# Kernel tuning notes

Hardware: AMD Instinct MI355X
Metric: run time of the kernel (lower is better)

The kernel has to match this reference:

```python
import jax, jax.numpy as jnp
import numpy as np

N, E, G = 50000, 1600000, 64
N_SPECIES, D_ATTR, D, N_RBF = 16, 16, 32, 8
CUTOFF = 5.0
SCALE, SHIFT = 1.0, 0.0


def setup_inputs() -> dict:
    key = jax.random.key(0)
    ks = jax.random.split(key, 20)

    def w(k, shape):
        fan_in = shape[-2] if len(shape) > 1 else shape[-1]
        return jax.random.normal(k, shape, dtype=jnp.float32) / np.sqrt(fan_in)

    return {
        "x": jax.random.randint(ks[0], (N, 1), 0, N_SPECIES),
        "pos": 3.0 * jax.random.normal(ks[1], (N, 3), dtype=jnp.float32),
        "edge_index": jax.random.randint(ks[2], (2, E), 0, N),
        "period_vec": 0.1 * jax.random.normal(ks[3], (E, 3), dtype=jnp.float32),
        "batch": jnp.sort(jax.random.randint(ks[4], (N,), 0, G)),
        "W_elem": w(ks[5], (N_SPECIES, D_ATTR)),
        "W0": w(ks[6], (D_ATTR, D)),
        "b0": jnp.zeros((D,), jnp.float32),
        "Wr1": w(ks[7], (3, N_RBF, D)),
        "br1": jnp.zeros((3, D), jnp.float32),
        "Wr2": w(ks[8], (3, D, D)),
        "Wmsg": w(ks[9], (3, D, D)),
        "Wattr": w(ks[10], (3, D_ATTR, D)),
        "Wself": w(ks[11], (3, D, D)),
        "bconv": jnp.zeros((3, D), jnp.float32),
        "wsh": w(ks[12], (3, 4)),
        "Wp1": w(ks[13], (D, 16)),
        "bp1": jnp.zeros((16,), jnp.float32),
        "Wp2": w(ks[14], (16, 1)),
        "bp2": jnp.zeros((1,), jnp.float32),
    }


def reference(x, pos, edge_index, period_vec, batch, W_elem, W0, b0, Wr1, br1,
              Wr2, Wmsg, Wattr, Wself, bconv, wsh, Wp1, bp1, Wp2, bp2):
    src, dst = edge_index[0], edge_index[1]

    # node_attr_layer: species embedding (gather), then first_atom_embed linear
    x_attr = W_elem[x[:, 0]]                              # [N, D_ATTR]
    h = x_attr @ W0 + b0                                  # [N, D]

    # edge_attr_layer: PBC edge vectors, lengths, l<=1 spherical harmonics
    edge_vec = pos[dst] - pos[src] + period_vec           # [E, 3]
    edge_len = jnp.linalg.norm(edge_vec, axis=-1, keepdims=True)  # [E, 1]
    unit = edge_vec / (edge_len + 1e-9)
    edge_sh = jnp.concatenate([jnp.ones_like(edge_len), unit], axis=-1)  # [E, 4]

    # edge_embedding_layer: Gaussian radial basis of edge lengths
    centers = jnp.linspace(0.0, CUTOFF, N_RBF, dtype=pos.dtype)
    gamma = jnp.asarray((N_RBF / CUTOFF) ** 2, pos.dtype)
    rbf = jnp.exp(-gamma * (edge_len - centers) ** 2)     # [E, N_RBF]

    # 3 conv layers: gather -> per-edge transform -> scatter-sum -> node update
    for i in range(3):
        rw = jax.nn.relu(rbf @ Wr1[i] + br1[i]) @ Wr2[i]  # [E, D] radial MLP
        sh_w = edge_sh @ wsh[i]                           # [E] sh mixing
        msg = (h[src] @ Wmsg[i]) * rw * sh_w[:, None]     # [E, D]
        agg = jax.ops.segment_sum(msg, dst, num_segments=N)  # [N, D]
        h = jax.nn.silu(agg + x_attr @ Wattr[i] + h @ Wself[i] + bconv[i])

    # post_conv layers
    h = jax.nn.silu(h @ Wp1 + bp1)                        # [N, 16]
    h = (h @ Wp2 + bp2)[:, 0]                             # [N] (squeeze)

    # scatter-sum pooling over graphs + affine energy scaling
    e = jax.ops.segment_sum(h, batch, num_segments=G)     # [G]
    return (e * SCALE + SHIFT)[:, None]                   # [G, 1]
```

## Files before the change

### kernel.cpp

```cpp
#include <hip/hip_runtime.h>
#include <hip/hip_fp16.h>
#include <math.h>

constexpr int N_NODES  = 50000;
constexpr int N_EDGES  = 1600000;
constexpr int G_GRAPHS = 64;
constexpr int D        = 32;
constexpr int D_ATTR   = 16;
constexpr int N_RBF    = 8;

constexpr int   TBL      = 8192;
constexpr int   TBL_ROWS = TBL + 1;
constexpr float LMAX     = 10.0f;

constexpr int BUCKET = 80;

constexpr int NT     = 64;
constexpr int NTILES = (N_NODES + NT - 1) / NT;
constexpr int TCAP   = 2432;
constexpr int EPB      = 2048;
constexpr int STHREADS = 512;
constexpr int EPV      = EPB / STHREADS;
constexpr int NBLK1    = (N_EDGES + EPB - 1) / EPB;

constexpr int NSLOT = NTILES * NT * BUCKET;

typedef unsigned int  uint4v  __attribute__((ext_vector_type(4)));
typedef unsigned int  uint2v  __attribute__((ext_vector_type(2)));

__device__ __forceinline__ float silu(float x) {
    return x / (1.0f + __expf(-x));
}
__device__ __forceinline__ float h2f_bits(unsigned short u) {
    return __half2float(__ushort_as_half(u));
}
__device__ __forceinline__ __half2 h2u(unsigned v) {
    union { unsigned u; __half2 h; } c; c.u = v; return c.h;
}

__global__ void node_init_kernel(const int* __restrict__ x,
                                 const float* __restrict__ W_elem,
                                 const float* __restrict__ W0,
                                 const float* __restrict__ b0,
                                 const float* __restrict__ Wmsg0,
                                 const float* __restrict__ Wself0,
                                 const float* __restrict__ Wattr,
                                 const float* __restrict__ bconv,
                                 __half* __restrict__ hm0,
                                 float* __restrict__ hs0,
                                 float* __restrict__ xa1,
                                 float* __restrict__ xa2,
                                 float* __restrict__ out) {
    int t = blockIdx.x * blockDim.x + threadIdx.x;
    if (t < G_GRAPHS) out[t] = 0.0f;
    int n = t >> 5, c = t & 31;
    if (n >= N_NODES) return;
    int sp = x[n];
    const float* we = W_elem + sp * D_ATTR;
    float xv = (c < D_ATTR) ? we[c] : 0.0f;
    float acc = b0[c];
#pragma unroll
    for (int a = 0; a < D_ATTR; ++a) acc += we[a] * W0[a * D + c];
    float m = 0.0f, s = 0.0f;
#pragma unroll
    for (int j = 0; j < D; ++j) {
        float hj = __shfl(acc, j, 32);
        m = fmaf(hj, Wmsg0[j * D + c], m);
        s = fmaf(hj, Wself0[j * D + c], s);
    }
    float a0 = bconv[0 * D + c], a1 = bconv[1 * D + c], a2 = bconv[2 * D + c];
#pragma unroll
    for (int j = 0; j < D_ATTR; ++j) {
        float xj = __shfl(xv, j, 32);
        a0 = fmaf(xj, Wattr[0 * D_ATTR * D + j * D + c], a0);
        a1 = fmaf(xj, Wattr[1 * D_ATTR * D + j * D + c], a1);
        a2 = fmaf(xj, Wattr[2 * D_ATTR * D + j * D + c], a2);
    }
    hm0[n * D + c] = __float2half(m);
    hs0[n * D + c] = s + a0;
    xa1[n * D + c] = a1;
    xa2[n * D + c] = a2;
}

__global__ __launch_bounds__(STHREADS) void hist_kernel(const int* __restrict__ eidx,
                                                        int* __restrict__ blk_hist) {
    __shared__ int hist[NTILES];
    int tid = threadIdx.x;
    int e0 = blockIdx.x * EPB;
    for (int i = tid; i < NTILES; i += STHREADS) hist[i] = 0;
    __syncthreads();
#pragma unroll
    for (int i = 0; i < EPV; ++i) {
        int e = e0 + tid + STHREADS * i;
        if (e < N_EDGES) atomicAdd(&hist[eidx[N_EDGES + e] >> 6], 1);
    }
    __syncthreads();
    int* dst = blk_hist + (size_t)blockIdx.x * NTILES;
    for (int t = tid; t < NTILES; t += STHREADS) dst[t] = hist[t];
}

__global__ void scan_kernel(const int* __restrict__ blk_hist,
                            int* __restrict__ blk_base,
                            int* __restrict__ tile_total) {
    int t = blockIdx.x;
    int lane = threadIdx.x;
    int run = 0;
    for (int b0 = 0; b0 < NBLK1; b0 += 64) {
        int b = b0 + lane;
        int v = (b < NBLK1) ? blk_hist[(size_t)b * NTILES + t] : 0;
        int pre = v;
#pragma unroll
        for (int o = 1; o < 64; o <<= 1) {
            int w = __shfl_up(pre, o);
            if (lane >= o) pre += w;
        }
        int excl = pre - v;
        if (b < NBLK1) blk_base[(size_t)b * NTILES + t] = run + excl;
        run += __shfl(pre, 63);
    }
    if (lane == 0) tile_total[t] = run;
}

__global__ __launch_bounds__(STHREADS) void scatter_kernel(const int* __restrict__ eidx,
                                                           const float* __restrict__ pos,
                                                           const float* __restrict__ period,
                                                           const float* __restrict__ wsh,
                                                           const int* __restrict__ blk_base,
                                                           uint4v* __restrict__ bins) {
    __shared__ int hist[NTILES];
    __shared__ int basev[NTILES];
    int tid = threadIdx.x;
    int e0 = blockIdx.x * EPB;
    const int* bb = blk_base + (size_t)blockIdx.x * NTILES;
    for (int i = tid; i < NTILES; i += STHREADS) {
        hist[i] = 0;
        basev[i] = bb[i];
    }
    __syncthreads();

    int   sarr[EPV], darr[EPV];
    float vx[EPV], vy[EPV], vz[EPV];
#pragma unroll
    for (int i = 0; i < EPV; ++i) {
        int e  = e0 + tid + STHREADS * i;
        int ec = (e < N_EDGES) ? e : (N_EDGES - 1);
        int s = eidx[ec];
        int d = eidx[N_EDGES + ec];
        sarr[i] = s;
        darr[i] = d;
        vx[i] = pos[d * 3 + 0] - pos[s * 3 + 0] + period[ec * 3 + 0];
        vy[i] = pos[d * 3 + 1] - pos[s * 3 + 1] + period[ec * 3 + 1];
        vz[i] = pos[d * 3 + 2] - pos[s * 3 + 2] + period[ec * 3 + 2];
    }
    asm volatile("" ::
        "v"(vx[0]), "v"(vx[1]), "v"(vx[2]), "v"(vx[3]),
        "v"(vy[0]), "v"(vy[1]), "v"(vy[2]), "v"(vy[3]),
        "v"(vz[0]), "v"(vz[1]), "v"(vz[2]), "v"(vz[3]),
        "v"(sarr[0]), "v"(sarr[1]), "v"(sarr[2]), "v"(sarr[3]),
        "v"(darr[0]), "v"(darr[1]), "v"(darr[2]), "v"(darr[3]));
#pragma unroll
    for (int i = 0; i < EPV; ++i) {
        int e = e0 + tid + STHREADS * i;
        if (e >= N_EDGES) continue;
        float len = sqrtf(vx[i] * vx[i] + vy[i] * vy[i] + vz[i] * vz[i]);
        float inv = 1.0f / (len + 1e-9f);
        int idx = (int)fminf(len * ((float)TBL / LMAX) + 0.5f, (float)TBL);
        float sw[3];
#pragma unroll
        for (int l = 0; l < 3; ++l)
            sw[l] = wsh[l * 4 + 0] +
                    (vx[i] * wsh[l * 4 + 1] + vy[i] * wsh[l * 4 + 2] + vz[i] * wsh[l * 4 + 3]) * inv;
        int tile = darr[i] >> 6;
        int rank = atomicAdd(&hist[tile], 1);
        int slot = basev[tile] + rank;
        if (slot < TCAP) {
            unsigned u0 = (unsigned)__half_as_ushort(__float2half(sw[0]));
            unsigned u1 = (unsigned)__half_as_ushort(__float2half(sw[1]));
            unsigned u2 = (unsigned)__half_as_ushort(__float2half(sw[2]));
            uint4v r;
            r.x = (unsigned)sarr[i] | ((unsigned)idx << 16);
            r.y = (unsigned)(darr[i] & (NT - 1));
            r.z = u0 | (u1 << 16);
            r.w = u2;
            bins[(size_t)tile * TCAP + slot] = r;
        }
    }
}

__global__ __launch_bounds__(512) void shuffle_kernel(const uint4v* __restrict__ bins,
                                                      const int* __restrict__ tile_total,
                                                      unsigned int* __restrict__ xs,
                                                      unsigned short* __restrict__ swp,
                                                      int* __restrict__ count) {
    __shared__ int lcur[NT];
    int tile = blockIdx.x;
    int tid = threadIdx.x;
    if (tid < NT) lcur[tid] = 0;
    __syncthreads();
    int cnt = tile_total[tile];
    if (cnt > TCAP) cnt = TCAP;
    const uint4v* base = bins + (size_t)tile * TCAP;
    for (int i = tid; i < cnt; i += 512) {
        uint4v r = __builtin_nontemporal_load(base + i);
        int dl = (int)(r.y & 63u);
        int slot = atomicAdd(&lcur[dl], 1);
        if (slot < BUCKET) {
            size_t g = (size_t)(tile * NT + dl) * BUCKET + slot;
            xs[g] = r.x;
            swp[0 * (size_t)NSLOT + g] = (unsigned short)(r.z & 0xFFFFu);
            swp[1 * (size_t)NSLOT + g] = (unsigned short)(r.z >> 16);
            swp[2 * (size_t)NSLOT + g] = (unsigned short)(r.w & 0xFFFFu);
        }
    }
    __syncthreads();
    if (tid < NT) {
        int node = tile * NT + tid;
        if (node < N_NODES) {
            int c = lcur[tid];
            count[node] = c < BUCKET ? c : BUCKET;
        }
    }
}

__global__ void table_kernel(const float* __restrict__ Wr1,
                             const float* __restrict__ br1,
                             const float* __restrict__ Wr2,
                             __half* __restrict__ table) {
    int t = blockIdx.x * blockDim.x + threadIdx.x;
    if (t >= 3 * TBL_ROWS) return;
    int l = t / TBL_ROWS;
    int idx = t % TBL_ROWS;
    float len = (float)idx * (LMAX / (float)TBL);
    const float gamma = (8.0f / 5.0f) * (8.0f / 5.0f);
    float rbf[N_RBF];
#pragma unroll
    for (int k = 0; k < N_RBF; ++k) {
        float dd = len - (float)k * (5.0f / 7.0f);
        rbf[k] = __expf(-gamma * dd * dd);
    }
    float out[D];
#pragma unroll
    for (int c = 0; c < D; ++c) out[c] = 0.0f;
    for (int j = 0; j < D; ++j) {
        float z = br1[l * D + j];
#pragma unroll
        for (int k = 0; k < N_RBF; ++k) z += rbf[k] * Wr1[l * N_RBF * D + k * D + j];
        z = fmaxf(z, 0.0f);
        const float* w2 = Wr2 + l * D * D + j * D;
#pragma unroll
        for (int c = 0; c < D; ++c) out[c] += z * w2[c];
    }
    __half* dst = table + ((size_t)(l * TBL_ROWS + idx)) * D;
#pragma unroll
    for (int c = 0; c < D; ++c) dst[c] = __float2half(out[c]);
}

template <int LAYER, bool NEXT>
__global__ __launch_bounds__(256, 5) void conv_kernel(const __half* __restrict__ hm,
                            const float* __restrict__ hs,
                            const unsigned int* __restrict__ xs,
                            const unsigned short* __restrict__ swp,
                            const int* __restrict__ count,
                            const __half* __restrict__ table,
                            const float* __restrict__ Wmsg_next,
                            const float* __restrict__ Wself_next,
                            const float* __restrict__ xa_next,
                            __half* __restrict__ hm_out,
                            float* __restrict__ hs_out,
                            float* __restrict__ h_final) {
    int wid = (blockIdx.x * blockDim.x + threadIdx.x) >> 6;
    int na = wid * 2;
    if (na >= N_NODES) return;
    int nb = na + 1;
    int lane = threadIdx.x & 63;
    int qw = lane >> 4;
    int q  = lane & 15;

    const unsigned* tab2 = (const unsigned*)(table + ((size_t)LAYER * TBL_ROWS) * D);
    const unsigned* hm2  = (const unsigned*)hm;
    const unsigned short* swb = swp + (size_t)LAYER * NSLOT;

    int cnta = count[na], cntb = count[nb];
    int bega = na * BUCKET, begb = nb * BUCKET;
    int enda = bega + cnta, endb = begb + cntb;
    int mx = cnta > cntb ? cnta : cntb;

    float axa = 0.0f, aya = 0.0f, axb = 0.0f, ayb = 0.0f;
    for (int k = 0; k < BUCKET; k += 32) {
        int o0a = bega + k + qw * 4, o1a = o0a + 16;
        int o0b = begb + k + qw * 4, o1b = o0b + 16;
        uint4v xa0 = __builtin_nontemporal_load((const uint4v*)(xs + o0a));
        uint4v xa1 = __builtin_nontemporal_load((const uint4v*)(xs + o1a));
        uint4v xb0 = __builtin_nontemporal_load((const uint4v*)(xs + o0b));
        uint4v xb1 = __builtin_nontemporal_load((const uint4v*)(xs + o1b));
        uint2v wa0 = __builtin_nontemporal_load((const uint2v*)(swb + o0a));
        uint2v wa1 = __builtin_nontemporal_load((const uint2v*)(swb + o1a));
        uint2v wb0 = __builtin_nontemporal_load((const uint2v*)(swb + o0b));
        uint2v wb1 = __builtin_nontemporal_load((const uint2v*)(swb + o1b));
        unsigned ua[8] = {xa0.x, xa0.y, xa0.z, xa0.w, xa1.x, xa1.y, xa1.z, xa1.w};
        unsigned ub[8] = {xb0.x, xb0.y, xb0.z, xb0.w, xb1.x, xb1.y, xb1.z, xb1.w};
        unsigned tva[8], mva[8], tvb[8], mvb[8];
#pragma unroll
        for (int j = 0; j < 8; ++j) {
            int slot = (j < 4) ? (o0a + j) : (o1a + j - 4);
            unsigned uu = (slot < enda) ? ua[j] : 0u;
            tva[j] = tab2[(int)(uu >> 16) * 16 + q];
            mva[j] = hm2[(int)(uu & 0xFFFFu) * 16 + q];
        }
#pragma unroll
        for (int j = 0; j < 8; ++j) {
            int slot = (j < 4) ? (o0b + j) : (o1b + j - 4);
            unsigned uu = (slot < endb) ? ub[j] : 0u;
            tvb[j] = tab2[(int)(uu >> 16) * 16 + q];
            mvb[j] = hm2[(int)(uu & 0xFFFFu) * 16 + q];
        }
        asm volatile("" ::
            "v"(tva[0]), "v"(tva[1]), "v"(tva[2]), "v"(tva[3]),
            "v"(tva[4]), "v"(tva[5]), "v"(tva[6]), "v"(tva[7]),
            "v"(mva[0]), "v"(mva[1]), "v"(mva[2]), "v"(mva[3]),
            "v"(mva[4]), "v"(mva[5]), "v"(mva[6]), "v"(mva[7]),
            "v"(tvb[0]), "v"(tvb[1]), "v"(tvb[2]), "v"(tvb[3]),
            "v"(tvb[4]), "v"(tvb[5]), "v"(tvb[6]), "v"(tvb[7]),
            "v"(mvb[0]), "v"(mvb[1]), "v"(mvb[2]), "v"(mvb[3]),
            "v"(mvb[4]), "v"(mvb[5]), "v"(mvb[6]), "v"(mvb[7]));
        unsigned short wva[8] = {
            (unsigned short)(wa0.x & 0xFFFFu), (unsigned short)(wa0.x >> 16),
            (unsigned short)(wa0.y & 0xFFFFu), (unsigned short)(wa0.y >> 16),
            (unsigned short)(wa1.x & 0xFFFFu), (unsigned short)(wa1.x >> 16),
            (unsigned short)(wa1.y & 0xFFFFu), (unsigned short)(wa1.y >> 16)};
        unsigned short wvb[8] = {
            (unsigned short)(wb0.x & 0xFFFFu), (unsigned short)(wb0.x >> 16),
            (unsigned short)(wb0.y & 0xFFFFu), (unsigned short)(wb0.y >> 16),
            (unsigned short)(wb1.x & 0xFFFFu), (unsigned short)(wb1.x >> 16),
            (unsigned short)(wb1.y & 0xFFFFu), (unsigned short)(wb1.y >> 16)};
#pragma unroll
        for (int j = 0; j < 8; ++j) {
            int slot = (j < 4) ? (o0a + j) : (o1a + j - 4);
            float sw = (slot < enda) ? h2f_bits(wva[j]) : 0.0f;
            float2 pf = __half22float2(__hmul2(h2u(tva[j]), h2u(mva[j])));
            axa = fmaf(pf.x, sw, axa);
            aya = fmaf(pf.y, sw, aya);
        }
#pragma unroll
        for (int j = 0; j < 8; ++j) {
            int slot = (j < 4) ? (o0b + j) : (o1b + j - 4);
            float sw = (slot < endb) ? h2f_bits(wvb[j]) : 0.0f;
            float2 pf = __half22float2(__hmul2(h2u(tvb[j]), h2u(mvb[j])));
            axb = fmaf(pf.x, sw, axb);
            ayb = fmaf(pf.y, sw, ayb);
        }
        if (k + 32 >= mx) break;
    }
    axa += __shfl_xor(axa, 16); axa += __shfl_xor(axa, 32);
    aya += __shfl_xor(aya, 16); aya += __shfl_xor(aya, 32);
    axb += __shfl_xor(axb, 16); axb += __shfl_xor(axb, 32);
    ayb += __shfl_xor(ayb, 16); ayb += __shfl_xor(ayb, 32);

    int c = lane & 31;
    float vxa = __shfl(axa, c >> 1), vya = __shfl(aya, c >> 1);
    float vxb = __shfl(axb, c >> 1), vyb = __shfl(ayb, c >> 1);
    float agga = (c & 1) ? vya : vxa;
    float aggb = (c & 1) ? vyb : vxb;
    bool hi = lane >= 32;
    int mynode = hi ? nb : na;
    float agg = hi ? aggb : agga;

    float hn = silu(agg + hs[mynode * D + c]);
    if (NEXT) {
        float m = 0.0f, s2 = 0.0f;
#pragma unroll
        for (int j = 0; j < D; ++j) {
            float hj = __shfl(hn, j, 32);
            m  = fmaf(hj, Wmsg_next[j * D + c], m);
            s2 = fmaf(hj, Wself_next[j * D + c], s2);
        }
        hm_out[mynode * D + c] = __float2half(m);
        hs_out[mynode * D + c] = s2 + xa_next[mynode * D + c];
    } else {
        h_final[mynode * D + c] = hn;
    }
}

__global__ void readout_kernel(const float* __restrict__ h,
                               const int* __restrict__ batch,
                               const float* __restrict__ Wp1,
                               const float* __restrict__ bp1,
                               const float* __restrict__ Wp2,
                               const float* __restrict__ bp2,
                               float* __restrict__ out) {
    int n = blockIdx.x * blockDim.x + threadIdx.x;
    float s = 0.0f;
    int b = -1;
    if (n < N_NODES) {
        b = batch[n];
        const float* hrow = h + n * D;
        float acc2 = bp2[0];
#pragma unroll
        for (int m = 0; m < 16; ++m) {
            float a = bp1[m];
#pragma unroll
            for (int j = 0; j < D; ++j) a += hrow[j] * Wp1[j * 16 + m];
            acc2 += silu(a) * Wp2[m];
        }
        s = acc2;
    }
    unsigned long long valid = __ballot(n < N_NODES);
    if (valid == 0ull) return;
    int firstLane = __ffsll(valid) - 1;
    int b0v = __shfl(b, firstLane);
    bool ok = (b == b0v) || (n >= N_NODES);
    if (__all(ok)) {
#pragma unroll
        for (int o = 32; o > 0; o >>= 1) s += __shfl_down(s, o);
        if ((threadIdx.x & 63) == 0) atomicAdd(out + b0v, s);
    } else {
        if (n < N_NODES) atomicAdd(out + b, s);
    }
}

extern "C" void kernel_launch(void* const* d_in, const int* in_sizes, int n_in,
                              void* d_out, int out_size, void* d_ws, size_t ws_size,
                              hipStream_t stream) {
    const int*   x      = (const int*)d_in[0];
    const float* pos    = (const float*)d_in[1];
    const int*   eidx   = (const int*)d_in[2];
    const float* period = (const float*)d_in[3];
    const int*   batch  = (const int*)d_in[4];
    const float* W_elem = (const float*)d_in[5];
    const float* W0     = (const float*)d_in[6];
    const float* b0     = (const float*)d_in[7];
    const float* Wr1    = (const float*)d_in[8];
    const float* br1    = (const float*)d_in[9];
    const float* Wr2    = (const float*)d_in[10];
    const float* Wmsg   = (const float*)d_in[11];
    const float* Wattr  = (const float*)d_in[12];
    const float* Wself  = (const float*)d_in[13];
    const float* bconv  = (const float*)d_in[14];
    const float* wsh    = (const float*)d_in[15];
    const float* Wp1    = (const float*)d_in[16];
    const float* bp1    = (const float*)d_in[17];
    const float* Wp2    = (const float*)d_in[18];
    const float* bp2    = (const float*)d_in[19];

    char* base = (char*)d_ws;
    size_t off = 0;
    auto carve = [&](size_t bytes) -> void* {
        void* p = base + off;
        off = (off + bytes + 255) & ~(size_t)255;
        return p;
    };
    __half*         hm_a        = (__half*)carve((size_t)N_NODES * D * 2);
    __half*         hm_b        = (__half*)carve((size_t)N_NODES * D * 2);
    float*          hs_a        = (float*)carve((size_t)N_NODES * D * 4);
    float*          hs_b        = (float*)carve((size_t)N_NODES * D * 4);
    float*          xa1         = (float*)carve((size_t)N_NODES * D * 4);
    float*          xa2         = (float*)carve((size_t)N_NODES * D * 4);
    float*          h_final     = (float*)carve((size_t)N_NODES * D * 4);
    unsigned int*   xs          = (unsigned int*)carve((size_t)NSLOT * 4);
    unsigned short* swp         = (unsigned short*)carve((size_t)3 * NSLOT * 2);
    uint4v*         bins        = (uint4v*)carve((size_t)NTILES * TCAP * 16);
    int*            blk_hist    = (int*)carve((size_t)NBLK1 * NTILES * 4);
    int*            blk_base    = (int*)carve((size_t)NBLK1 * NTILES * 4);
    int*            tile_total  = (int*)carve((size_t)NTILES * 4);
    int*            count       = (int*)carve((size_t)NTILES * NT * 4);
    __half*         table       = (__half*)carve((size_t)3 * TBL_ROWS * D * 2);
    (void)ws_size; (void)in_sizes; (void)n_in; (void)out_size;

    node_init_kernel<<<(N_NODES * 32 + 255) / 256, 256, 0, stream>>>(
        x, W_elem, W0, b0, Wmsg + 0 * D * D, Wself + 0 * D * D, Wattr, bconv,
        hm_a, hs_a, xa1, xa2, (float*)d_out);
    hist_kernel<<<NBLK1, STHREADS, 0, stream>>>(eidx, blk_hist);
    scan_kernel<<<NTILES, 64, 0, stream>>>(blk_hist, blk_base, tile_total);
    scatter_kernel<<<NBLK1, STHREADS, 0, stream>>>(eidx, pos, period, wsh, blk_base, bins);
    table_kernel<<<(3 * TBL_ROWS + 127) / 128, 128, 0, stream>>>(Wr1, br1, Wr2, table);
    shuffle_kernel<<<NTILES, 512, 0, stream>>>(bins, tile_total, xs, swp, count);

    int cwaves = (N_NODES + 1) / 2;
    int cgrid  = (cwaves * 64 + 255) / 256;
    conv_kernel<0, true><<<cgrid, 256, 0, stream>>>(
        hm_a, hs_a, xs, swp, count, table, Wmsg + 1 * D * D, Wself + 1 * D * D, xa1,
        hm_b, hs_b, nullptr);
    conv_kernel<1, true><<<cgrid, 256, 0, stream>>>(
        hm_b, hs_b, xs, swp, count, table, Wmsg + 2 * D * D, Wself + 2 * D * D, xa2,
        hm_a, hs_a, nullptr);
    conv_kernel<2, false><<<cgrid, 256, 0, stream>>>(
        hm_a, hs_a, xs, swp, count, table, nullptr, nullptr, nullptr,
        nullptr, nullptr, h_final);

    readout_kernel<<<(N_NODES + 255) / 256, 256, 0, stream>>>(h_final, batch, Wp1, bp1, Wp2, bp2,
                                                              (float*)d_out);
}
```

Measured before the change: 388.8 us.

## Gather table and node rows with 16-byte loads, four lanes per edge

Restructures the conv gather so each lane loads a 16-byte chunk of the table row and the message row (four lanes per edge, sixteen edges per pass) instead of 4-byte chunks with sixteen lanes per edge. Each lane now keeps eight accumulators, reduced by a shuffle tree and combined through shared memory with a block barrier. The aim is fewer, wider memory transactions per edge. In exchange it needs more registers, lowered by relaxing launch bounds from 5 to 4 blocks, and adds a __syncthreads that sits after an early return for out-of-range warps.

```diff
diff --git a/kernel.cpp b/kernel.cpp
--- a/kernel.cpp
+++ b/kernel.cpp
@@ -36,6 +36,17 @@
 }
 __device__ __forceinline__ __half2 h2u(unsigned v) {
     union { unsigned u; __half2 h; } c; c.u = v; return c.h;
+}
+
+__device__ __forceinline__ void accum8(uint4v t, uint4v m, float sw, float (&acc)[8]) {
+    float2 p0 = __half22float2(__hmul2(h2u(t.x), h2u(m.x)));
+    float2 p1 = __half22float2(__hmul2(h2u(t.y), h2u(m.y)));
+    float2 p2 = __half22float2(__hmul2(h2u(t.z), h2u(m.z)));
+    float2 p3 = __half22float2(__hmul2(h2u(t.w), h2u(m.w)));
+    acc[0] = fmaf(p0.x, sw, acc[0]); acc[1] = fmaf(p0.y, sw, acc[1]);
+    acc[2] = fmaf(p1.x, sw, acc[2]); acc[3] = fmaf(p1.y, sw, acc[3]);
+    acc[4] = fmaf(p2.x, sw, acc[4]); acc[5] = fmaf(p2.y, sw, acc[5]);
+    acc[6] = fmaf(p3.x, sw, acc[6]); acc[7] = fmaf(p3.y, sw, acc[7]);
 }
 
 __global__ void node_init_kernel(const int* __restrict__ x,
@@ -256,7 +267,7 @@
 }
 
 template <int LAYER, bool NEXT>
-__global__ __launch_bounds__(256, 5) void conv_kernel(const __half* __restrict__ hm,
+__global__ __launch_bounds__(256, 4) void conv_kernel(const __half* __restrict__ hm,
                             const float* __restrict__ hs,
                             const unsigned int* __restrict__ xs,
                             const unsigned short* __restrict__ swp,
@@ -268,102 +279,81 @@
                             __half* __restrict__ hm_out,
                             float* __restrict__ hs_out,
                             float* __restrict__ h_final) {
+    __shared__ float sagg[4][2][32];
     int wid = (blockIdx.x * blockDim.x + threadIdx.x) >> 6;
     int na = wid * 2;
     if (na >= N_NODES) return;
     int nb = na + 1;
     int lane = threadIdx.x & 63;
-    int qw = lane >> 4;
-    int q  = lane & 15;
-
-    const unsigned* tab2 = (const unsigned*)(table + ((size_t)LAYER * TBL_ROWS) * D);
-    const unsigned* hm2  = (const unsigned*)hm;
+    int w  = (threadIdx.x >> 6) & 3;
+    int rg = lane >> 2;
+    int cg = lane & 3;
+
+    const uint4v* tab4 = (const uint4v*)(table + (size_t)LAYER * TBL_ROWS * D);
+    const uint4v* hm4  = (const uint4v*)hm;
     const unsigned short* swb = swp + (size_t)LAYER * NSLOT;
 
     int cnta = count[na], cntb = count[nb];
     int bega = na * BUCKET, begb = nb * BUCKET;
-    int enda = bega + cnta, endb = begb + cntb;
     int mx = cnta > cntb ? cnta : cntb;
 
-    float axa = 0.0f, aya = 0.0f, axb = 0.0f, ayb = 0.0f;
+    float acca[8], accb[8];
+#pragma unroll
+    for (int j = 0; j < 8; ++j) { acca[j] = 0.0f; accb[j] = 0.0f; }
+
     for (int k = 0; k < BUCKET; k += 32) {
-        int o0a = bega + k + qw * 4, o1a = o0a + 16;
-        int o0b = begb + k + qw * 4, o1b = o0b + 16;
-        uint4v xa0 = __builtin_nontemporal_load((const uint4v*)(xs + o0a));
-        uint4v xa1 = __builtin_nontemporal_load((const uint4v*)(xs + o1a));
-        uint4v xb0 = __builtin_nontemporal_load((const uint4v*)(xs + o0b));
-        uint4v xb1 = __builtin_nontemporal_load((const uint4v*)(xs + o1b));
-        uint2v wa0 = __builtin_nontemporal_load((const uint2v*)(swb + o0a));
-        uint2v wa1 = __builtin_nontemporal_load((const uint2v*)(swb + o1a));
-        uint2v wb0 = __builtin_nontemporal_load((const uint2v*)(swb + o0b));
-        uint2v wb1 = __builtin_nontemporal_load((const uint2v*)(swb + o1b));
-        unsigned ua[8] = {xa0.x, xa0.y, xa0.z, xa0.w, xa1.x, xa1.y, xa1.z, xa1.w};
-        unsigned ub[8] = {xb0.x, xb0.y, xb0.z, xb0.w, xb1.x, xb1.y, xb1.z, xb1.w};
-        unsigned tva[8], mva[8], tvb[8], mvb[8];
+        int r0 = k + rg, r1 = k + 16 + rg;
+        bool va0 = r0 < cnta, va1 = r1 < cnta;
+        bool vb0 = r0 < cntb, vb1 = r1 < cntb;
+        unsigned ua0 = va0 ? xs[bega + r0] : 0u;
+        unsigned ua1 = va1 ? xs[bega + r1] : 0u;
+        unsigned ub0 = vb0 ? xs[begb + r0] : 0u;
+        unsigned ub1 = vb1 ? xs[begb + r1] : 0u;
+        float sa0 = va0 ? h2f_bits(swb[bega + r0]) : 0.0f;
+        float sa1 = va1 ? h2f_bits(swb[bega + r1]) : 0.0f;
+        float sb0 = vb0 ? h2f_bits(swb[begb + r0]) : 0.0f;
+        float sb1 = vb1 ? h2f_bits(swb[begb + r1]) : 0.0f;
+        uint4v ta0 = tab4[(size_t)(ua0 >> 16) * 4 + cg];
+        uint4v ma0 = hm4[(size_t)(ua0 & 0xFFFFu) * 4 + cg];
+        uint4v ta1 = tab4[(size_t)(ua1 >> 16) * 4 + cg];
+        uint4v ma1 = hm4[(size_t)(ua1 & 0xFFFFu) * 4 + cg];
+        uint4v tb0 = tab4[(size_t)(ub0 >> 16) * 4 + cg];
+        uint4v mb0 = hm4[(size_t)(ub0 & 0xFFFFu) * 4 + cg];
+        uint4v tb1 = tab4[(size_t)(ub1 >> 16) * 4 + cg];
+        uint4v mb1 = hm4[(size_t)(ub1 & 0xFFFFu) * 4 + cg];
+        asm volatile("" :: "v"(ta0.x), "v"(ma0.x), "v"(ta1.x), "v"(ma1.x),
+                           "v"(tb0.x), "v"(mb0.x), "v"(tb1.x), "v"(mb1.x));
+        accum8(ta0, ma0, sa0, acca);
+        accum8(ta1, ma1, sa1, acca);
+        accum8(tb0, mb0, sb0, accb);
+        accum8(tb1, mb1, sb1, accb);
+        if (k + 32 >= mx) break;
+    }
+
+#pragma unroll
+    for (int j = 0; j < 8; ++j) {
+        acca[j] += __shfl_xor(acca[j], 4);
+        acca[j] += __shfl_xor(acca[j], 8);
+        acca[j] += __shfl_xor(acca[j], 16);
+        acca[j] += __shfl_xor(acca[j], 32);
+        accb[j] += __shfl_xor(accb[j], 4);
+        accb[j] += __shfl_xor(accb[j], 8);
+        accb[j] += __shfl_xor(accb[j], 16);
+        accb[j] += __shfl_xor(accb[j], 32);
+    }
+    if (rg == 0) {
 #pragma unroll
         for (int j = 0; j < 8; ++j) {
-            int slot = (j < 4) ? (o0a + j) : (o1a + j - 4);
-            unsigned uu = (slot < enda) ? ua[j] : 0u;
-            tva[j] = tab2[(int)(uu >> 16) * 16 + q];
-            mva[j] = hm2[(int)(uu & 0xFFFFu) * 16 + q];
-        }
-#pragma unroll
-        for (int j = 0; j < 8; ++j) {
-            int slot = (j < 4) ? (o0b + j) : (o1b + j - 4);
-            unsigned uu = (slot < endb) ? ub[j] : 0u;
-            tvb[j] = tab2[(int)(uu >> 16) * 16 + q];
-            mvb[j] = hm2[(int)(uu & 0xFFFFu) * 16 + q];
-        }
-        asm volatile("" ::
-            "v"(tva[0]), "v"(tva[1]), "v"(tva[2]), "v"(tva[3]),
-            "v"(tva[4]), "v"(tva[5]), "v"(tva[6]), "v"(tva[7]),
-            "v"(mva[0]), "v"(mva[1]), "v"(mva[2]), "v"(mva[3]),
-            "v"(mva[4]), "v"(mva[5]), "v"(mva[6]), "v"(mva[7]),
-            "v"(tvb[0]), "v"(tvb[1]), "v"(tvb[2]), "v"(tvb[3]),
-            "v"(tvb[4]), "v"(tvb[5]), "v"(tvb[6]), "v"(tvb[7]),
-            "v"(mvb[0]), "v"(mvb[1]), "v"(mvb[2]), "v"(mvb[3]),
-            "v"(mvb[4]), "v"(mvb[5]), "v"(mvb[6]), "v"(mvb[7]));
-        unsigned short wva[8] = {
-            (unsigned short)(wa0.x & 0xFFFFu), (unsigned short)(wa0.x >> 16),
-            (unsigned short)(wa0.y & 0xFFFFu), (unsigned short)(wa0.y >> 16),
-            (unsigned short)(wa1.x & 0xFFFFu), (unsigned short)(wa1.x >> 16),
-            (unsigned short)(wa1.y & 0xFFFFu), (unsigned short)(wa1.y >> 16)};
-        unsigned short wvb[8] = {
-            (unsigned short)(wb0.x & 0xFFFFu), (unsigned short)(wb0.x >> 16),
-            (unsigned short)(wb0.y & 0xFFFFu), (unsigned short)(wb0.y >> 16),
-            (unsigned short)(wb1.x & 0xFFFFu), (unsigned short)(wb1.x >> 16),
-            (unsigned short)(wb1.y & 0xFFFFu), (unsigned short)(wb1.y >> 16)};
-#pragma unroll
-        for (int j = 0; j < 8; ++j) {
-            int slot = (j < 4) ? (o0a + j) : (o1a + j - 4);
-            float sw = (slot < enda) ? h2f_bits(wva[j]) : 0.0f;
-            float2 pf = __half22float2(__hmul2(h2u(tva[j]), h2u(mva[j])));
-            axa = fmaf(pf.x, sw, axa);
-            aya = fmaf(pf.y, sw, aya);
-        }
-#pragma unroll
-        for (int j = 0; j < 8; ++j) {
-            int slot = (j < 4) ? (o0b + j) : (o1b + j - 4);
-            float sw = (slot < endb) ? h2f_bits(wvb[j]) : 0.0f;
-            float2 pf = __half22float2(__hmul2(h2u(tvb[j]), h2u(mvb[j])));
-            axb = fmaf(pf.x, sw, axb);
-            ayb = fmaf(pf.y, sw, ayb);
-        }
-        if (k + 32 >= mx) break;
-    }
-    axa += __shfl_xor(axa, 16); axa += __shfl_xor(axa, 32);
-    aya += __shfl_xor(aya, 16); aya += __shfl_xor(aya, 32);
-    axb += __shfl_xor(axb, 16); axb += __shfl_xor(axb, 32);
-    ayb += __shfl_xor(ayb, 16); ayb += __shfl_xor(ayb, 32);
+            sagg[w][0][cg * 8 + j] = acca[j];
+            sagg[w][1][cg * 8 + j] = accb[j];
+        }
+    }
+    __syncthreads();
 
     int c = lane & 31;
-    float vxa = __shfl(axa, c >> 1), vya = __shfl(aya, c >> 1);
-    float vxb = __shfl(axb, c >> 1), vyb = __shfl(ayb, c >> 1);
-    float agga = (c & 1) ? vya : vxa;
-    float aggb = (c & 1) ? vyb : vxb;
-    bool hi = lane >= 32;
+    int hi = lane >> 5;
     int mynode = hi ? nb : na;
-    float agg = hi ? aggb : agga;
+    float agg = sagg[w][hi][c];
 
     float hn = silu(agg + hs[mynode * D + c]);
     if (NEXT) {
```

Measured after the change: 374.3 us. 1.04x faster.
